# Kernel tuning notes

Measured on AMD Instinct MI355X. Metric: run time of the kernel, lower is better.

Reference implementation:

```python
import jax, jax.numpy as jnp
import numpy as np

E = 768   # embed_dim
N = 12    # num_heads
H = 128   # height
W = 128   # width
D = E // N  # head_dim = 64


def setup_inputs() -> dict:
    key = jax.random.key(0)
    ks = jax.random.split(key, 9)
    s = 0.02
    x = jax.random.normal(ks[0], (1, H * W, E), jnp.float32)
    Wq = jax.random.normal(ks[1], (E, E), jnp.float32) * s
    bq = jnp.zeros((E,), jnp.float32)
    Wk = jax.random.normal(ks[2], (E, E), jnp.float32) * s
    bk = jnp.zeros((E,), jnp.float32)
    Wv = jax.random.normal(ks[3], (E, E), jnp.float32) * s
    bv = jnp.zeros((E,), jnp.float32)
    Wo = jax.random.normal(ks[4], (E, E), jnp.float32) * s
    bo = jnp.zeros((E,), jnp.float32)
    return {"x": x, "Wq": Wq, "bq": bq, "Wk": Wk, "bk": bk,
            "Wv": Wv, "bv": bv, "Wo": Wo, "bo": bo}


def reference(x, Wq, bq, Wk, bk, Wv, bv, Wo, bo):
    # projections (torch Linear: x @ W.T + b)
    q = x @ Wq.T + bq
    k = x @ Wk.T + bk
    v = x @ Wv.T + bv

    # q, k -> (1, N, H, W, D)
    q = q.reshape(1, H, W, N, D).transpose(0, 3, 1, 2, 4)
    k = k.reshape(1, H, W, N, D).transpose(0, 3, 1, 2, 4)

    # --- width-axis attention (per row h) ---
    qr_w = q.transpose(0, 2, 1, 3, 4)  # (1, H, N, W, D)
    kr_w = k.transpose(0, 2, 1, 3, 4)  # (1, H, N, W, D)
    v = v.reshape(1, H, W, N, D).transpose(0, 1, 3, 2, 4)  # (1, H, N, W, D)
    # NOTE: original applies no 1/sqrt(D) scaling
    qk_w = jnp.einsum('bhnwd,bhnvd->bhnwv', qr_w, kr_w)  # (1, H, N, W, W)
    qk_w = jax.nn.softmax(qk_w, axis=-1)
    v = jnp.einsum('bhnwv,bhnvd->bhnwd', qk_w, v)  # (1, H, N, W, D)

    # --- height-axis attention (per column w) ---
    qr_h = q.transpose(0, 3, 1, 2, 4)  # (1, W, N, H, D)
    kr_h = k.transpose(0, 3, 1, 2, 4)  # (1, W, N, H, D)
    v = v.transpose(0, 3, 2, 1, 4)     # (1, W, N, H, D)
    qk_h = jnp.einsum('bwnhd,bwngd->bwnhg', qr_h, kr_h)  # (1, W, N, H, H)
    qk_h = jax.nn.softmax(qk_h, axis=-1)
    out = jnp.einsum('bwnhg,bwngd->bwnhd', qk_h, v)  # (1, W, N, H, D)

    # (1, W, N, H, D) -> (1, H, W, N, D) -> (1, H, W, E)
    out = out.transpose(0, 3, 1, 2, 4).reshape(1, H, W, E)
    out = out @ Wo.T + bo
    return out.reshape(1, H * W, E)
```

## Files before the change

### kernel.cpp

```cpp
#include <hip/hip_runtime.h>

typedef __attribute__((ext_vector_type(4))) float f32x4;
typedef __attribute__((ext_vector_type(8))) unsigned short u16x8;
typedef __attribute__((ext_vector_type(8))) __bf16 bf16x8;

typedef __attribute__((address_space(3))) unsigned lds_u32;
typedef const __attribute__((address_space(1))) unsigned glb_u32;

__device__ __forceinline__ unsigned short f2bf(float f) {
    union { float f; unsigned u; } v; v.f = f;
    unsigned r = v.u + 0x7fffu + ((v.u >> 16) & 1u);
    return (unsigned short)(r >> 16);
}

__device__ __forceinline__ f32x4 mfma16(u16x8 a, u16x8 b, f32x4 c) {
    return __builtin_amdgcn_mfma_f32_16x16x32_bf16(
        __builtin_bit_cast(bf16x8, a), __builtin_bit_cast(bf16x8, b), c, 0, 0, 0);
}

__device__ __forceinline__ void gload16(const unsigned short* g, unsigned short* l) {
    __builtin_amdgcn_global_load_lds((glb_u32*)g, (lds_u32*)l, 16, 0, 0);
}

#define BARM() asm volatile("s_barrier" ::: "memory")
#define WAITVM0() asm volatile("s_waitcnt vmcnt(0)" ::: "memory")

__global__ void cvt_f32_bf16(const float* __restrict__ src,
                             unsigned short* __restrict__ dst, int n) {
    int stride = gridDim.x * blockDim.x * 4;
    for (int i = (blockIdx.x * blockDim.x + threadIdx.x) * 4; i < n; i += stride) {
        float4 f = *reinterpret_cast<const float4*>(src + i);
        ushort4 o;
        o.x = f2bf(f.x); o.y = f2bf(f.y); o.z = f2bf(f.z); o.w = f2bf(f.w);
        *reinterpret_cast<ushort4*>(dst + i) = o;
    }
}

__global__ void cvt4_f32_bf16(const float* __restrict__ s0, const float* __restrict__ s1,
                              const float* __restrict__ s2, const float* __restrict__ s3,
                              unsigned short* __restrict__ dst, int per) {
    int total = per * 4;
    int stride = gridDim.x * blockDim.x * 4;
    for (int i = (blockIdx.x * blockDim.x + threadIdx.x) * 4; i < total; i += stride) {
        int w = i / per, off = i - w * per;
        const float* s = w == 0 ? s0 : w == 1 ? s1 : w == 2 ? s2 : s3;
        float4 f = *reinterpret_cast<const float4*>(s + off);
        ushort4 o;
        o.x = f2bf(f.x); o.y = f2bf(f.y); o.z = f2bf(f.z); o.w = f2bf(f.w);
        *reinterpret_cast<ushort4*>(dst + i) = o;
    }
}

template<bool OUTF32>
__global__ __launch_bounds__(256, 2) void gemm128(
    const unsigned short* __restrict__ A,
    const unsigned short* __restrict__ B,
    const float* __restrict__ b0, const float* __restrict__ b1, const float* __restrict__ b2,
    void* __restrict__ C0, void* __restrict__ C1, void* __restrict__ C2,
    int K, int NBY)
{
    __shared__ char lds[65536];
    const int t = threadIdx.x, lane = t & 63, wave = t >> 6;
    const int wm = wave >> 1, wn = wave & 1;

    const int nwg = gridDim.x;
    const int bid = blockIdx.x;
    const int swzb = (bid & 7) * (nwg >> 3) + (bid >> 3);
    const long m0 = (long)(swzb / NBY) * 128;
    const long n0 = (long)(swzb % NBY) * 128;

    const int NT = K >> 6;

    const int rloc = t >> 3;
    const int cel  = ((t & 7) ^ ((t >> 3) & 7)) << 3;
    const unsigned short* Ab = A + (m0 + rloc) * (long)K + cel;
    const unsigned short* Bb = B + (n0 + rloc) * (long)K + cel;

    auto STAGE = [&](int kt) {
        char* da = lds + ((kt & 1) << 14) + (wave << 10);
        char* db = lds + 32768 + ((kt & 1) << 14) + (wave << 10);
        const unsigned short* sa = Ab + kt * 64;
        const unsigned short* sb = Bb + kt * 64;
        #pragma unroll
        for (int j = 0; j < 4; ++j) {
            gload16(sa + (long)(j * 32) * K, (unsigned short*)(da + j * 4096));
            gload16(sb + (long)(j * 32) * K, (unsigned short*)(db + j * 4096));
        }
    };

    f32x4 acc[4][4] = {};
    u16x8 af[4][2], bf[4][2];

    auto LD = [&](int slot) {
        const char* bufA = lds + (slot << 14);
        const char* bufB = lds + 32768 + (slot << 14);
        #pragma unroll
        for (int f = 0; f < 4; ++f)
            #pragma unroll
            for (int kk = 0; kk < 2; ++kk) {
                int ra = wm * 64 + f * 16 + (lane & 15);
                int rb = wn * 64 + f * 16 + (lane & 15);
                int cb = kk * 64 + (lane >> 4) * 16;
                af[f][kk] = *(const u16x8*)(bufA + ra * 128 + (cb ^ ((ra & 7) << 4)));
                bf[f][kk] = *(const u16x8*)(bufB + rb * 128 + (cb ^ ((rb & 7) << 4)));
            }
    };

    STAGE(0);
    WAITVM0();
    BARM();

    for (int kt = 0; kt < NT; ++kt) {
        int nx = kt + 1;
        if (nx >= NT) nx = NT - 2;
        STAGE(nx);
        LD(kt & 1);
        #pragma unroll
        for (int kk = 0; kk < 2; ++kk)
            #pragma unroll
            for (int mi = 0; mi < 4; ++mi)
                #pragma unroll
                for (int nf = 0; nf < 4; ++nf)
                    acc[mi][nf] = mfma16(af[mi][kk], bf[nf][kk], acc[mi][nf]);
        WAITVM0();
        BARM();
    }

    #pragma unroll
    for (int mi = 0; mi < 4; ++mi)
        #pragma unroll
        for (int nf = 0; nf < 4; ++nf) {
            int coln = (int)n0 + wn * 64 + nf * 16 + (lane & 15);
            int which = coln / 768;
            int nl = coln - which * 768;
            const float* bs = which == 0 ? b0 : (which == 1 ? b1 : b2);
            void* Cp       = which == 0 ? C0 : (which == 1 ? C1 : C2);
            float bias = bs[nl];
            #pragma unroll
            for (int q = 0; q < 4; ++q) {
                long row = m0 + wm * 64 + mi * 16 + ((lane >> 4) << 2) + q;
                float val = acc[mi][nf][q] + bias;
                if (OUTF32) ((float*)Cp)[row * 768 + nl] = val;
                else ((unsigned short*)Cp)[row * 768 + nl] = f2bf(val);
            }
        }
}

__global__ __launch_bounds__(256, 3) void attn128(
    const unsigned short* __restrict__ Q,
    const unsigned short* __restrict__ K,
    const unsigned short* __restrict__ V,
    unsigned short* __restrict__ O,
    int mult, int stride)
{
    __shared__ unsigned short QK[2][128][72];
    __shared__ unsigned short Vst[64][136];
    unsigned short (*Qs)[72] = QK[0];
    unsigned short (*Ks)[72] = QK[1];
    unsigned short (*Ps)[136] = (unsigned short (*)[136])&QK[0][0][0];

    const int pos = blockIdx.x, head = blockIdx.y;
    const int t = threadIdx.x, wave = t >> 6, lane = t & 63;

    for (int p = 0; p < 4; ++p) {
        int f = p * 2048 + t * 8;
        int r = f >> 6;
        int d = f & 63;
        long g = ((long)(pos * mult + r * stride)) * 768 + head * 64 + d;
        *(u16x8*)&Qs[r][d] = *(const u16x8*)&Q[g];
        *(u16x8*)&Ks[r][d] = *(const u16x8*)&K[g];
        u16x8 vv = *(const u16x8*)&V[g];
        #pragma unroll
        for (int j = 0; j < 8; ++j) Vst[d + j][r] = vv[j];
    }
    __syncthreads();

    const int rb = wave * 32;
    f32x4 s[2][8] = {};
    #pragma unroll
    for (int d0 = 0; d0 < 64; d0 += 32) {
        u16x8 a[2], b[8];
        #pragma unroll
        for (int mi = 0; mi < 2; ++mi)
            a[mi] = *(const u16x8*)&Qs[rb + mi * 16 + (lane & 15)][d0 + (lane >> 4) * 8];
        #pragma unroll
        for (int ni = 0; ni < 8; ++ni)
            b[ni] = *(const u16x8*)&Ks[ni * 16 + (lane & 15)][d0 + (lane >> 4) * 8];
        #pragma unroll
        for (int mi = 0; mi < 2; ++mi)
            #pragma unroll
            for (int ni = 0; ni < 8; ++ni)
                s[mi][ni] = mfma16(a[mi], b[ni], s[mi][ni]);
    }
    __syncthreads();

    #pragma unroll
    for (int mi = 0; mi < 2; ++mi) {
        #pragma unroll
        for (int q = 0; q < 4; ++q) {
            float m = -1e30f;
            #pragma unroll
            for (int ni = 0; ni < 8; ++ni) m = fmaxf(m, s[mi][ni][q]);
            m = fmaxf(m, __shfl_xor(m, 1));
            m = fmaxf(m, __shfl_xor(m, 2));
            m = fmaxf(m, __shfl_xor(m, 4));
            m = fmaxf(m, __shfl_xor(m, 8));
            float p[8], sum = 0.f;
            #pragma unroll
            for (int ni = 0; ni < 8; ++ni) { p[ni] = __expf(s[mi][ni][q] - m); sum += p[ni]; }
            sum += __shfl_xor(sum, 1);
            sum += __shfl_xor(sum, 2);
            sum += __shfl_xor(sum, 4);
            sum += __shfl_xor(sum, 8);
            float inv = 1.0f / sum;
            int row = rb + mi * 16 + ((lane >> 4) << 2) + q;
            #pragma unroll
            for (int ni = 0; ni < 8; ++ni)
                Ps[row][ni * 16 + (lane & 15)] = f2bf(p[ni] * inv);
        }
    }
    __syncthreads();

    f32x4 o[2][4] = {};
    #pragma unroll
    for (int v0 = 0; v0 < 128; v0 += 32) {
        u16x8 a[2], b[4];
        #pragma unroll
        for (int mi = 0; mi < 2; ++mi)
            a[mi] = *(const u16x8*)&Ps[rb + mi * 16 + (lane & 15)][v0 + (lane >> 4) * 8];
        #pragma unroll
        for (int ni = 0; ni < 4; ++ni)
            b[ni] = *(const u16x8*)&Vst[ni * 16 + (lane & 15)][v0 + (lane >> 4) * 8];
        #pragma unroll
        for (int mi = 0; mi < 2; ++mi)
            #pragma unroll
            for (int ni = 0; ni < 4; ++ni)
                o[mi][ni] = mfma16(a[mi], b[ni], o[mi][ni]);
    }

    #pragma unroll
    for (int mi = 0; mi < 2; ++mi)
        #pragma unroll
        for (int ni = 0; ni < 4; ++ni)
            #pragma unroll
            for (int q = 0; q < 4; ++q) {
                int row = rb + mi * 16 + ((lane >> 4) << 2) + q;
                int col = ni * 16 + (lane & 15);
                long g = ((long)(pos * mult + row * stride)) * 768 + head * 64 + col;
                O[g] = f2bf(o[mi][ni][q]);
            }
}

extern "C" void kernel_launch(void* const* d_in, const int* in_sizes, int n_in,
                              void* d_out, int out_size, void* d_ws, size_t ws_size,
                              hipStream_t stream) {
    const float* x  = (const float*)d_in[0];
    const float* Wq = (const float*)d_in[1];
    const float* bq = (const float*)d_in[2];
    const float* Wk = (const float*)d_in[3];
    const float* bk = (const float*)d_in[4];
    const float* Wv = (const float*)d_in[5];
    const float* bv = (const float*)d_in[6];
    const float* Wo = (const float*)d_in[7];
    const float* bo = (const float*)d_in[8];
    float* out = (float*)d_out;

    const size_t MS = (size_t)16384 * 768;
    const size_t WS = (size_t)768 * 768;
    unsigned short* xb   = (unsigned short*)d_ws;
    unsigned short* Qb   = xb + MS;
    unsigned short* Kb   = Qb + MS;
    unsigned short* Vb   = Kb + MS;
    unsigned short* Wqkv = Vb + MS;
    unsigned short* Wob  = Wqkv + 3 * WS;

    cvt_f32_bf16<<<2048, 256, 0, stream>>>(x, xb, (int)MS);
    cvt4_f32_bf16<<<2304, 256, 0, stream>>>(Wq, Wk, Wv, Wo, Wqkv, (int)WS);

    gemm128<false><<<2304, 256, 0, stream>>>(
        xb, Wqkv, bq, bk, bv, Qb, Kb, Vb, 768, 18);

    attn128<<<dim3(128, 12), 256, 0, stream>>>(Qb, Kb, Vb, xb, 128, 1);
    attn128<<<dim3(128, 12), 256, 0, stream>>>(Qb, Kb, xb, Vb, 1, 128);

    gemm128<true><<<768, 256, 0, stream>>>(
        Vb, Wob, bo, bo, bo, out, out, out, 768, 6);
}
```

Before: 182.3 us.

## Drop GEMM double buffering to halve LDS and raise occupancy

Converts the GEMM kernel into a shared device core with single-buffered LDS (32KB instead of 64KB). Each k-tile is now loaded, waited on, then computed, instead of prefetching the next tile during MFMA. Launch bounds rise from 2 to 4 blocks per CU, aiming to hide memory latency through occupancy rather than software pipelining. The cost is an exposed load wait and an extra barrier every k-iteration, plus tighter register limits.

```diff
diff --git a/kernel.cpp b/kernel.cpp
--- a/kernel.cpp
+++ b/kernel.cpp
@@ -52,14 +52,14 @@
 }
 
 template<bool OUTF32>
-__global__ __launch_bounds__(256, 2) void gemm128(
+__device__ __forceinline__ void gemm_core(
     const unsigned short* __restrict__ A,
     const unsigned short* __restrict__ B,
     const float* __restrict__ b0, const float* __restrict__ b1, const float* __restrict__ b2,
     void* __restrict__ C0, void* __restrict__ C1, void* __restrict__ C2,
     int K, int NBY)
 {
-    __shared__ char lds[65536];
+    __shared__ char lds[32768];
     const int t = threadIdx.x, lane = t & 63, wave = t >> 6;
     const int wm = wave >> 1, wn = wave & 1;
 
@@ -77,8 +77,8 @@
     const unsigned short* Bb = B + (n0 + rloc) * (long)K + cel;
 
     auto STAGE = [&](int kt) {
-        char* da = lds + ((kt & 1) << 14) + (wave << 10);
-        char* db = lds + 32768 + ((kt & 1) << 14) + (wave << 10);
+        char* da = lds + (wave << 10);
+        char* db = lds + 16384 + (wave << 10);
         const unsigned short* sa = Ab + kt * 64;
         const unsigned short* sb = Bb + kt * 64;
         #pragma unroll
@@ -89,11 +89,11 @@
     };
 
     f32x4 acc[4][4] = {};
-    u16x8 af[4][2], bf[4][2];
-
-    auto LD = [&](int slot) {
-        const char* bufA = lds + (slot << 14);
-        const char* bufB = lds + 32768 + (slot << 14);
+    u16x8 af[4][2], bfr[4][2];
+
+    auto LD = [&]() {
+        const char* bufA = lds;
+        const char* bufB = lds + 16384;
         #pragma unroll
         for (int f = 0; f < 4; ++f)
             #pragma unroll
@@ -101,28 +101,23 @@
                 int ra = wm * 64 + f * 16 + (lane & 15);
                 int rb = wn * 64 + f * 16 + (lane & 15);
                 int cb = kk * 64 + (lane >> 4) * 16;
-                af[f][kk] = *(const u16x8*)(bufA + ra * 128 + (cb ^ ((ra & 7) << 4)));
-                bf[f][kk] = *(const u16x8*)(bufB + rb * 128 + (cb ^ ((rb & 7) << 4)));
+                af[f][kk]  = *(const u16x8*)(bufA + ra * 128 + (cb ^ ((ra & 7) << 4)));
+                bfr[f][kk] = *(const u16x8*)(bufB + rb * 128 + (cb ^ ((rb & 7) << 4)));
             }
     };
 
-    STAGE(0);
-    WAITVM0();
-    BARM();
-
     for (int kt = 0; kt < NT; ++kt) {
-        int nx = kt + 1;
-        if (nx >= NT) nx = NT - 2;
-        STAGE(nx);
-        LD(kt & 1);
+        STAGE(kt);
+        WAITVM0();
+        BARM();
+        LD();
         #pragma unroll
         for (int kk = 0; kk < 2; ++kk)
             #pragma unroll
             for (int mi = 0; mi < 4; ++mi)
                 #pragma unroll
                 for (int nf = 0; nf < 4; ++nf)
-                    acc[mi][nf] = mfma16(af[mi][kk], bf[nf][kk], acc[mi][nf]);
-        WAITVM0();
+                    acc[mi][nf] = mfma16(af[mi][kk], bfr[nf][kk], acc[mi][nf]);
         BARM();
     }
 
@@ -144,6 +139,22 @@
                 else ((unsigned short*)Cp)[row * 768 + nl] = f2bf(val);
             }
         }
+}
+
+__global__ __launch_bounds__(256, 4) void qkv_gemm(
+    const unsigned short* __restrict__ A, const unsigned short* __restrict__ B,
+    const float* b0, const float* b1, const float* b2,
+    void* C0, void* C1, void* C2, int K, int NBY)
+{
+    gemm_core<false>(A, B, b0, b1, b2, C0, C1, C2, K, NBY);
+}
+
+__global__ __launch_bounds__(256, 4) void oproj_gemm(
+    const unsigned short* __restrict__ A, const unsigned short* __restrict__ B,
+    const float* b0, const float* b1, const float* b2,
+    void* C0, void* C1, void* C2, int K, int NBY)
+{
+    gemm_core<true>(A, B, b0, b1, b2, C0, C1, C2, K, NBY);
 }
 
 __global__ __launch_bounds__(256, 3) void attn128(
@@ -277,12 +288,12 @@
     cvt_f32_bf16<<<2048, 256, 0, stream>>>(x, xb, (int)MS);
     cvt4_f32_bf16<<<2304, 256, 0, stream>>>(Wq, Wk, Wv, Wo, Wqkv, (int)WS);
 
-    gemm128<false><<<2304, 256, 0, stream>>>(
+    qkv_gemm<<<2304, 256, 0, stream>>>(
         xb, Wqkv, bq, bk, bv, Qb, Kb, Vb, 768, 18);
 
     attn128<<<dim3(128, 12), 256, 0, stream>>>(Qb, Kb, Vb, xb, 128, 1);
     attn128<<<dim3(128, 12), 256, 0, stream>>>(Qb, Kb, xb, Vb, 1, 128);
 
-    gemm128<true><<<768, 256, 0, stream>>>(
+    oproj_gemm<<<768, 256, 0, stream>>>(
         Vb, Wob, bo, bo, bo, out, out, out, 768, 6);
 }
```

New measurement: 169.3 us. -7.2%, faster.
